# Kernel optimization log

Measured on AMD Instinct MI355X. Metric: run time of the kernel, lower is better.

The kernel has to match this reference:

```python
import jax, jax.numpy as jnp
import numpy as np

N_NODES = 50000


def gcn_conv(x, src, dst, W, b, n_nodes):
    """PyG GCNConv: linear -> sym-normalized aggregation with self-loops -> bias."""
    h = x @ W  # [N, out]
    # add self loops
    loop = jnp.arange(n_nodes, dtype=src.dtype)
    src_f = jnp.concatenate([src, loop])
    dst_f = jnp.concatenate([dst, loop])
    # degree at target nodes (edge weight = 1)
    deg = jax.ops.segment_sum(jnp.ones_like(dst_f, dtype=h.dtype), dst_f, num_segments=n_nodes)
    dinv = jnp.where(deg > 0, jax.lax.rsqrt(deg), 0.0)
    norm = dinv[src_f] * dinv[dst_f]  # [E+N]
    msg = h[src_f] * norm[:, None]    # gather + scale
    out = jax.ops.segment_sum(msg, dst_f, num_segments=n_nodes)
    return out + b


def setup_inputs() -> dict:
    key = jax.random.key(0)
    k1, k2, k3, k4 = jax.random.split(key, 4)
    N, F, H, C, E = N_NODES, 512, 256, 16, 800000
    x = jax.random.normal(k1, (N, F), dtype=jnp.float32)
    edge_index = jax.random.randint(k2, (2, E), 0, N, dtype=jnp.int64)
    W1 = jax.random.normal(k3, (F, H), dtype=jnp.float32) * (1.0 / np.sqrt(F))
    b1 = jnp.zeros((H,), dtype=jnp.float32)
    W2 = jax.random.normal(k4, (H, C), dtype=jnp.float32) * (1.0 / np.sqrt(H))
    b2 = jnp.zeros((C,), dtype=jnp.float32)
    return {"x": x, "edge_index": edge_index, "W1": W1, "b1": b1, "W2": W2, "b2": b2}


def reference(x, edge_index, W1, b1, W2, b2):
    src, dst = edge_index[0], edge_index[1]
    h = gcn_conv(x, src, dst, W1, b1, N_NODES)
    h = jax.nn.relu(h)
    # F.dropout with training=False (eval mode) is identity
    out = gcn_conv(h, src, dst, W2, b2, N_NODES)
    return out
```

## Files before the change

### kernel.cpp

```cpp
#include <hip/hip_runtime.h>
#include <stdint.h>

#define N_NODES 50000
#define N_PAD   50048
#define F_IN 512
#define H_DIM 256
#define C_DIM 16

typedef __attribute__((ext_vector_type(8))) short short8;
typedef __attribute__((ext_vector_type(4))) float f32x4;
typedef __attribute__((ext_vector_type(2))) float f32x2;
typedef __attribute__((ext_vector_type(4))) unsigned short us4;
typedef __attribute__((ext_vector_type(8))) unsigned short us8;

__device__ inline float bf2f(unsigned short u) {
    return __uint_as_float(((uint32_t)u) << 16);
}
__device__ inline unsigned short f2bf(float f) {
    uint32_t u = __float_as_uint(f);
    u += 0x7FFFu + ((u >> 16) & 1u);
    return (unsigned short)(u >> 16);
}
__device__ inline unsigned short hx(float f) {
    return (unsigned short)(__float_as_uint(f) >> 16);
}
__device__ inline int eidx(const void* p, long long i, int is64) {
    return is64 ? (int)((const long long*)p)[i] : ((const int*)p)[i];
}

#if __has_builtin(__builtin_amdgcn_cvt_pk_fp8_f32)
__device__ inline uint8_t f2fp8(float f) {
    int r = __builtin_amdgcn_cvt_pk_fp8_f32(f, f, 0, false);
    return (uint8_t)(r & 0xFF);
}
#else
__device__ inline uint8_t f2fp8(float f) {
    uint32_t u = __float_as_uint(f);
    uint32_t s = (u >> 24) & 0x80u;
    float a = fabsf(f);
    if (a >= 448.f) return (uint8_t)(s | 0x7E);
    if (a < 0.015625f) {
        int d = (int)rintf(a * 512.f);
        if (d < 8) return (uint8_t)(s | d);
        return (uint8_t)(s | 0x08);
    }
    uint32_t au = u & 0x7FFFFFFFu;
    uint32_t r = au + 0x7FFFFu + ((au >> 20) & 1u);
    uint32_t e = (r >> 23) - 120u;
    uint32_t m = (r >> 20) & 7u;
    if (e > 15u || (e == 15u && m == 7u)) return (uint8_t)(s | 0x7E);
    return (uint8_t)(s | (e << 3) | m);
}
#endif

#if __has_builtin(__builtin_amdgcn_cvt_pk_f32_fp8)
#define FP8CVT(w, hi) __builtin_amdgcn_cvt_pk_f32_fp8((w), (hi))
#else
__device__ inline float fp8b_to_f32(uint32_t v) {
    uint32_t e = (v >> 3) & 0xF, m = v & 7, s = (v >> 7) & 1;
    float r = e ? __uint_as_float(((e + 120u) << 23) | (m << 20))
                : (float)m * 0.001953125f;
    return s ? -r : r;
}
__device__ inline f32x2 FP8CVT(uint32_t w, bool hi) {
    uint32_t b = hi ? (w >> 16) : w;
    f32x2 r;
    r.x = fp8b_to_f32(b & 0xFF);
    r.y = fp8b_to_f32((b >> 8) & 0xFF);
    return r;
}
#endif

__device__ inline int row_beg(const int* ro, const int* bs, int n) {
    return ro[n] + bs[n >> 9];
}
__device__ inline int row_end(const int* ro, const int* bs, int n, int E) {
    return (n + 1 < N_NODES) ? ro[n + 1] + bs[(n + 1) >> 9] : E;
}

#define GLOAD16(gp, lp)                                                       \
    __builtin_amdgcn_global_load_lds(                                         \
        (const __attribute__((address_space(1))) void*)(gp),                  \
        (__attribute__((address_space(3))) void*)(lp), 16, 0, 0)


__global__ void prep_k(const void* ei, int* flag,
                       const float* w1, unsigned short* w1t,
                       const float* w2, unsigned short* w2t,
                       int* cnt, int* cur) {
    int i = blockIdx.x * 256 + threadIdx.x;
    if (i == 0) {
        const uint32_t* w = (const uint32_t*)ei;
        int is64 = 1;
        for (int j = 1; j < 128; j += 2)
            if (w[j] != 0u) { is64 = 0; break; }
        *flag = is64;
    }
    if (i < N_NODES) { cnt[i] = 0; cur[i] = 0; }
    if (i < F_IN * H_DIM) {
        int k = i / H_DIM, n = i % H_DIM;
        w1t[n * F_IN + k] = f2bf(w1[i]);
    }
    if (i < H_DIM * C_DIM) {
        int k = i / C_DIM, n = i % C_DIM;
        w2t[n * H_DIM + k] = f2bf(w2[i]);
    }
}


__global__ void hist_k(const void* ei, const int* flag, int* cnt, long long E) {
    long long e = (long long)blockIdx.x * 256 + threadIdx.x;
    if (e >= E) return;
    int d = eidx(ei, E + e, *flag);
    atomicAdd(&cnt[d], 1);
}

__global__ __launch_bounds__(512) void scan1_k(const int* cnt, int* rowoff, int* bsum,
                                               float* dinv, int n) {
    __shared__ int s[512];
    int t = threadIdx.x;
    int i = blockIdx.x * 512 + t;
    int v = (i < n) ? cnt[i] : 0;
    s[t] = v;
    __syncthreads();
    for (int off = 1; off < 512; off <<= 1) {
        int add = (t >= off) ? s[t - off] : 0;
        __syncthreads();
        s[t] += add;
        __syncthreads();
    }
    if (i < n) {
        rowoff[i] = s[t] - v;
        dinv[i] = rsqrtf((float)(v + 1));
    }
    if (t == 511) bsum[blockIdx.x] = s[511];
}

__global__ void scan2_k(int* bsum, int nb) {
    __shared__ int s[128];
    int t = threadIdx.x;
    int v = (t < nb) ? bsum[t] : 0;
    s[t] = v;
    __syncthreads();
    for (int off = 1; off < 128; off <<= 1) {
        int add = (t >= off) ? s[t - off] : 0;
        __syncthreads();
        s[t] += add;
        __syncthreads();
    }
    if (t < nb) bsum[t] = s[t] - v;
}

__global__ void scatter_k(const void* ei, const int* flag, const float* dinv,
                          const int* rowoff, const int* bsum, int* cur,
                          long long E, int2* colnorm) {
    long long e = (long long)blockIdx.x * 256 + threadIdx.x;
    if (e >= E) return;
    int is64 = *flag;
    int s = eidx(ei, e, is64);
    int d = eidx(ei, E + e, is64);
    int pos = row_beg(rowoff, bsum, d) + atomicAdd(&cur[d], 1);
    float nrm = dinv[s] * dinv[d];
    int2 cn;
    cn.x = s;
    cn.y = __float_as_int(nrm);
    colnorm[pos] = cn;
}


__global__ __launch_bounds__(512, 4) void gemm1_k(const float* __restrict__ x,
                                                  const unsigned short* __restrict__ w1t,
                                                  uint8_t* __restrict__ h1) {
    __shared__ __align__(16) float          Asf[2][128 * 32];
    __shared__ __align__(16) unsigned short Bs[2][256 * 32];

    const int t = threadIdx.x;
    const int wv = t >> 6, lane = t & 63;
    const int lg = lane >> 4, lr = lane & 15;
    const int wm = wv >> 2, wn = wv & 3;

    const int arow0 = t >> 3;
    const int achk = (t & 7) ^ (arow0 & 7);
    size_t g0 = (size_t)blockIdx.x * 128 + arow0;
    size_t g1 = g0 + 64;
    if (g0 > N_NODES - 1) g0 = N_NODES - 1;
    if (g1 > N_NODES - 1) g1 = N_NODES - 1;
    const float* asrc0 = x + g0 * F_IN + achk * 4;
    const float* asrc1 = x + g1 * F_IN + achk * 4;
    const unsigned short* bsrc0 = w1t + (size_t)(t >> 2) * F_IN + (t & 3) * 8;
    const unsigned short* bsrc1 = bsrc0 + 128 * F_IN;

#define STAGE(bf, ks)                                                         \
    do { const int _o = (ks) * 32;                                            \
        GLOAD16(asrc0 + _o, &Asf[bf][t * 4]);                                 \
        GLOAD16(asrc1 + _o, &Asf[bf][t * 4 + 2048]);                          \
        GLOAD16(bsrc0 + _o, &Bs[bf][t * 8]);                                  \
        GLOAD16(bsrc1 + _o, &Bs[bf][(t + 512) * 8]);                          \
    } while (0)

    f32x4 acc[4][4] = {};

    STAGE(0, 0);

    for (int ks = 0; ks < 16; ++ks) {
        const int bf = ks & 1;
        if (ks < 15) {
            STAGE(bf ^ 1, ks + 1);
            asm volatile("s_waitcnt vmcnt(4)" ::: "memory");
        } else {
            asm volatile("s_waitcnt vmcnt(0)" ::: "memory");
        }
        __builtin_amdgcn_sched_barrier(0);
        __builtin_amdgcn_s_barrier();

        short8 afr[4], bfr[4];
#pragma unroll
        for (int mi = 0; mi < 4; ++mi) {
            const int r = wm * 64 + mi * 16 + lr;
            const int s = r & 7;
            const float* base = &Asf[bf][r * 32];
            f32x4 lo = *(const f32x4*)(base + (((lg * 2) ^ s) * 4));
            f32x4 hi = *(const f32x4*)(base + (((lg * 2 + 1) ^ s) * 4));
            short8 a;
            a[0] = (short)hx(lo[0]); a[1] = (short)hx(lo[1]);
            a[2] = (short)hx(lo[2]); a[3] = (short)hx(lo[3]);
            a[4] = (short)hx(hi[0]); a[5] = (short)hx(hi[1]);
            a[6] = (short)hx(hi[2]); a[7] = (short)hx(hi[3]);
            afr[mi] = a;
        }
#pragma unroll
        for (int ni = 0; ni < 4; ++ni)
            bfr[ni] = *(const short8*)&Bs[bf][(wn * 64 + ni * 16 + lr) * 32 + lg * 8];
#pragma unroll
        for (int mi = 0; mi < 4; ++mi)
#pragma unroll
            for (int ni = 0; ni < 4; ++ni)
                acc[mi][ni] = __builtin_amdgcn_mfma_f32_16x16x32_bf16(
                    afr[mi], bfr[ni], acc[mi][ni], 0, 0, 0);

        asm volatile("s_waitcnt lgkmcnt(0)" ::: "memory");
        __builtin_amdgcn_sched_barrier(0);
        __builtin_amdgcn_s_barrier();
    }
#undef STAGE

    const size_t rbase = (size_t)blockIdx.x * 128 + wm * 64 + lg * 4;
#pragma unroll
    for (int mi = 0; mi < 4; ++mi)
#pragma unroll
        for (int ni = 0; ni < 4; ++ni) {
            const int col = wn * 64 + ni * 16 + lr;
#pragma unroll
            for (int j = 0; j < 4; ++j)
                h1[(rbase + mi * 16 + j) * H_DIM + col] = f2fp8(acc[mi][ni][j]);
        }
}


__global__ __launch_bounds__(256) void agg1_k(const uint8_t* __restrict__ h1,
                                              const int* __restrict__ rowoff,
                                              const int* __restrict__ bsum,
                                              const int2* __restrict__ colnorm,
                                              const float* __restrict__ dinv,
                                              const float* __restrict__ b1,
                                              unsigned short* __restrict__ h1a,
                                              int E) {
    int wv = threadIdx.x >> 6, lane = threadIdx.x & 63;
    int node = blockIdx.x * 4 + wv;
    if (node >= N_NODES) return;
    int half = lane >> 5;
    int fl = (lane & 31) * 8;
    int beg = row_beg(rowoff, bsum, node);
    int end = row_end(rowoff, bsum, node, E);
    float a[8] = {0.f, 0.f, 0.f, 0.f, 0.f, 0.f, 0.f, 0.f};
    const uint8_t* base = h1 + fl;

#define ACCUM(vv, nn)                                                         \
    do { f32x2 p0 = FP8CVT((vv).x, false), p1 = FP8CVT((vv).x, true);         \
         f32x2 p2 = FP8CVT((vv).y, false), p3 = FP8CVT((vv).y, true);         \
         a[0] += (nn) * p0.x; a[1] += (nn) * p0.y;                            \
         a[2] += (nn) * p1.x; a[3] += (nn) * p1.y;                            \
         a[4] += (nn) * p2.x; a[5] += (nn) * p2.y;                            \
         a[6] += (nn) * p3.x; a[7] += (nn) * p3.y; } while (0)

    int e = beg + half;
    while (e + 6 < end) {
        int2 c[4];
        uint2 v[4];
#pragma unroll
        for (int q = 0; q < 4; ++q) c[q] = colnorm[e + q * 2];
#pragma unroll
        for (int q = 0; q < 4; ++q)
            v[q] = *(const uint2*)(base + (size_t)c[q].x * H_DIM);
#pragma unroll
        for (int q = 0; q < 4; ++q) {
            float n = __int_as_float(c[q].y);
            ACCUM(v[q], n);
        }
        e += 8;
    }
    while (e < end) {
        int2 c0 = colnorm[e];
        uint2 v0 = *(const uint2*)(base + (size_t)c0.x * H_DIM);
        float n0 = __int_as_float(c0.y);
        ACCUM(v0, n0);
        e += 2;
    }
#undef ACCUM
#pragma unroll
    for (int j = 0; j < 8; ++j)
        a[j] += __shfl_xor(a[j], 32);

    if (half == 0) {
        float dn = dinv[node];
        float sn = dn * dn;
        uint2 vsv = *(const uint2*)(base + (size_t)node * H_DIM);
        f32x2 s0 = FP8CVT(vsv.x, false), s1 = FP8CVT(vsv.x, true);
        f32x2 s2 = FP8CVT(vsv.y, false), s3 = FP8CVT(vsv.y, true);
        float sv[8] = {s0.x, s0.y, s1.x, s1.y, s2.x, s2.y, s3.x, s3.y};
        float4 b0 = *(const float4*)(b1 + fl);
        float4 b4 = *(const float4*)(b1 + fl + 4);
        float bb[8] = {b0.x, b0.y, b0.z, b0.w, b4.x, b4.y, b4.z, b4.w};
        us8 o;
#pragma unroll
        for (int j = 0; j < 8; ++j) {
            float r = fmaxf(a[j] + sn * sv[j] + bb[j], 0.f);
            o[j] = f2bf(r);
        }
        *(us8*)(h1a + (long long)node * H_DIM + fl) = o;
    }
}


__global__ __launch_bounds__(256) void gemm2_k(const unsigned short* __restrict__ h1a,
                                               const unsigned short* __restrict__ w2t,
                                               float* __restrict__ h2) {
    int t = threadIdx.x;
    int wv = t >> 6, lane = t & 63, lg = lane >> 4, lr = lane & 15;
    int rbase = blockIdx.x * 64 + wv * 16;
    int rr = rbase + lr;
    int rc = rr < N_NODES ? rr : N_NODES - 1;
    f32x4 acc = {0.f, 0.f, 0.f, 0.f};
#pragma unroll
    for (int ks = 0; ks < 8; ++ks) {
        short8 a = *(const short8*)(h1a + (long long)rc * H_DIM + ks * 32 + lg * 8);
        short8 b = *(const short8*)(w2t + lr * H_DIM + ks * 32 + lg * 8);
        acc = __builtin_amdgcn_mfma_f32_16x16x32_bf16(a, b, acc, 0, 0, 0);
    }
#pragma unroll
    for (int j = 0; j < 4; ++j) {
        int row = rbase + lg * 4 + j;
        if (row < N_NODES) h2[(long long)row * C_DIM + lr] = acc[j];
    }
}


__global__ __launch_bounds__(256) void agg2_k(const float* __restrict__ h2,
                                              const int* __restrict__ rowoff,
                                              const int* __restrict__ bsum,
                                              const int2* __restrict__ colnorm,
                                              const float* __restrict__ dinv,
                                              const float* __restrict__ b2,
                                              float* __restrict__ out, int E) {
    int g = threadIdx.x >> 4, c = threadIdx.x & 15;
    int node = blockIdx.x * 16 + g;
    if (node >= N_NODES) return;
    int beg = row_beg(rowoff, bsum, node);
    int end = row_end(rowoff, bsum, node, E);
    float acc = 0.f;
    int e = beg;
    for (; e + 3 < end; e += 4) {
        int2 cn0 = colnorm[e];
        int2 cn1 = colnorm[e + 1];
        int2 cn2 = colnorm[e + 2];
        int2 cn3 = colnorm[e + 3];
        float v0 = h2[(long long)cn0.x * C_DIM + c];
        float v1 = h2[(long long)cn1.x * C_DIM + c];
        float v2 = h2[(long long)cn2.x * C_DIM + c];
        float v3 = h2[(long long)cn3.x * C_DIM + c];
        acc += __int_as_float(cn0.y) * v0 + __int_as_float(cn1.y) * v1
             + __int_as_float(cn2.y) * v2 + __int_as_float(cn3.y) * v3;
    }
    for (; e < end; ++e) {
        int2 cn = colnorm[e];
        acc += __int_as_float(cn.y) * h2[(long long)cn.x * C_DIM + c];
    }
    float dn = dinv[node];
    acc += dn * dn * h2[(long long)node * C_DIM + c];
    out[(long long)node * C_DIM + c] = acc + b2[c];
}


extern "C" void kernel_launch(void* const* d_in, const int* in_sizes, int n_in,
                              void* d_out, int out_size, void* d_ws, size_t ws_size,
                              hipStream_t stream) {
    const float* x  = (const float*)d_in[0];
    const void*  ei = d_in[1];
    const float* W1 = (const float*)d_in[2];
    const float* b1 = (const float*)d_in[3];
    const float* W2 = (const float*)d_in[4];
    const float* b2 = (const float*)d_in[5];
    float* out = (float*)d_out;
    long long E = (long long)in_sizes[1] / 2;

    char* w = (char*)d_ws;
    auto alloc = [&](size_t bytes) -> char* {
        char* p = w;
        w += (bytes + 255) & ~(size_t)255;
        return p;
    };
    int*   flag    = (int*)   alloc(4);
    int*   cnt     = (int*)   alloc((size_t)N_NODES * 4);
    int*   cur     = (int*)   alloc((size_t)N_NODES * 4);
    float* dinv    = (float*) alloc((size_t)N_NODES * 4);
    int*   rowoff  = (int*)   alloc((size_t)N_NODES * 4);
    int*   bsum    = (int*)   alloc(512 * 4);
    int2*  colnorm = (int2*)  alloc((size_t)E * 8);
    unsigned short* w1t = (unsigned short*)alloc((size_t)H_DIM * F_IN * 2);
    unsigned short* w2t = (unsigned short*)alloc((size_t)C_DIM * H_DIM * 2);
    uint8_t* h1 = (uint8_t*)alloc((size_t)N_PAD * H_DIM);
    unsigned short* h1a = (unsigned short*)alloc((size_t)N_NODES * H_DIM * 2);
    float* h2 = (float*)alloc((size_t)N_NODES * C_DIM * 4);

    prep_k<<<(F_IN * H_DIM + 255) / 256, 256, 0, stream>>>(ei, flag, W1, w1t, W2, w2t,
                                                           cnt, cur);

    int egrid = (int)((E + 255) / 256);
    hist_k<<<egrid, 256, 0, stream>>>(ei, flag, cnt, E);
    int sgrid = (N_NODES + 511) / 512;
    scan1_k<<<sgrid, 512, 0, stream>>>(cnt, rowoff, bsum, dinv, N_NODES);
    scan2_k<<<1, 128, 0, stream>>>(bsum, sgrid);
    scatter_k<<<egrid, 256, 0, stream>>>(ei, flag, dinv, rowoff, bsum, cur, E, colnorm);

    gemm1_k<<<N_PAD / 128, 512, 0, stream>>>(x, w1t, h1);
    agg1_k<<<(N_NODES + 3) / 4, 256, 0, stream>>>(h1, rowoff, bsum, colnorm, dinv,
                                                  b1, h1a, (int)E);
    gemm2_k<<<(N_NODES + 63) / 64, 256, 0, stream>>>(h1a, w2t, h2);
    agg2_k<<<(N_NODES + 15) / 16, 256, 0, stream>>>(h2, rowoff, bsum, colnorm, dinv,
                                                    b2, out, (int)E);
}
```

Before: 181.4 us.

## Fold block-sum scan into scatter, process two edges per thread, widen agg2 per node

Removes the separate single-block scan2 launch by having every scatter block redo the small 98-entry block-sum scan in shared memory, with block 0 writing the exclusive result to a new bscan buffer that the aggregation kernels read. The hist and scatter kernels now handle two edges per thread, halving their grids. agg2 moves from 16 lanes per node to a full wavefront per node, splitting edges across four lane groups and combining them with shuffles. This trades redundant per-block scan work and lower node-per-block density in agg2 for one fewer launch and more memory-level parallelism on high-degree rows.

```diff
diff --git a/kernel.cpp b/kernel.cpp
--- a/kernel.cpp
+++ b/kernel.cpp
@@ -6,6 +6,7 @@
 #define F_IN 512
 #define H_DIM 256
 #define C_DIM 16
+#define NCHUNK ((N_NODES + 511) / 512)
 
 typedef __attribute__((ext_vector_type(8))) short short8;
 typedef __attribute__((ext_vector_type(4))) float f32x4;
@@ -109,10 +110,12 @@
 
 
 __global__ void hist_k(const void* ei, const int* flag, int* cnt, long long E) {
-    long long e = (long long)blockIdx.x * 256 + threadIdx.x;
+    long long e = ((long long)blockIdx.x * 256 + threadIdx.x) * 2;
     if (e >= E) return;
-    int d = eidx(ei, E + e, *flag);
-    atomicAdd(&cnt[d], 1);
+    int is64 = *flag;
+    atomicAdd(&cnt[eidx(ei, E + e, is64)], 1);
+    if (e + 1 < E)
+        atomicAdd(&cnt[eidx(ei, E + e + 1, is64)], 1);
 }
 
 __global__ __launch_bounds__(512) void scan1_k(const int* cnt, int* rowoff, int* bsum,
@@ -136,35 +139,44 @@
     if (t == 511) bsum[blockIdx.x] = s[511];
 }
 
-__global__ void scan2_k(int* bsum, int nb) {
-    __shared__ int s[128];
-    int t = threadIdx.x;
-    int v = (t < nb) ? bsum[t] : 0;
-    s[t] = v;
+
+__global__ __launch_bounds__(256) void scatter_k(const void* ei, const int* flag,
+                                                 const float* dinv,
+                                                 const int* rowoff, const int* bsum,
+                                                 int* bscan, int* cur,
+                                                 long long E, int2* colnorm) {
+    __shared__ int sb[128];
+    const int t = threadIdx.x;
+    if (t < 128) sb[t] = (t < NCHUNK) ? bsum[t] : 0;
     __syncthreads();
+#pragma unroll
     for (int off = 1; off < 128; off <<= 1) {
-        int add = (t >= off) ? s[t - off] : 0;
+        int add = (t < 128 && t >= off) ? sb[t - off] : 0;
         __syncthreads();
-        s[t] += add;
+        if (t < 128) sb[t] += add;
         __syncthreads();
     }
-    if (t < nb) bsum[t] = s[t] - v;
-}
-
-__global__ void scatter_k(const void* ei, const int* flag, const float* dinv,
-                          const int* rowoff, const int* bsum, int* cur,
-                          long long E, int2* colnorm) {
-    long long e = (long long)blockIdx.x * 256 + threadIdx.x;
-    if (e >= E) return;
-    int is64 = *flag;
-    int s = eidx(ei, e, is64);
-    int d = eidx(ei, E + e, is64);
-    int pos = row_beg(rowoff, bsum, d) + atomicAdd(&cur[d], 1);
-    float nrm = dinv[s] * dinv[d];
-    int2 cn;
-    cn.x = s;
-    cn.y = __float_as_int(nrm);
-    colnorm[pos] = cn;
+    int ex = 0;
+    if (t < 128) ex = (t == 0) ? 0 : sb[t - 1];
+    __syncthreads();
+    if (t < 128) sb[t] = ex;
+    __syncthreads();
+    if (blockIdx.x == 0 && t < NCHUNK) bscan[t] = sb[t];
+
+    const int is64 = *flag;
+    long long e = ((long long)blockIdx.x * 256 + t) * 2;
+#pragma unroll
+    for (int q = 0; q < 2; ++q, ++e) {
+        if (e >= E) break;
+        int s = eidx(ei, e, is64);
+        int d = eidx(ei, E + e, is64);
+        int pos = rowoff[d] + sb[d >> 9] + atomicAdd(&cur[d], 1);
+        float nrm = dinv[s] * dinv[d];
+        int2 cn;
+        cn.x = s;
+        cn.y = __float_as_int(nrm);
+        colnorm[pos] = cn;
+    }
 }
 
 
@@ -259,7 +271,7 @@
 
 __global__ __launch_bounds__(256) void agg1_k(const uint8_t* __restrict__ h1,
                                               const int* __restrict__ rowoff,
-                                              const int* __restrict__ bsum,
+                                              const int* __restrict__ bscan,
                                               const int2* __restrict__ colnorm,
                                               const float* __restrict__ dinv,
                                               const float* __restrict__ b1,
@@ -270,8 +282,8 @@
     if (node >= N_NODES) return;
     int half = lane >> 5;
     int fl = (lane & 31) * 8;
-    int beg = row_beg(rowoff, bsum, node);
-    int end = row_end(rowoff, bsum, node, E);
+    int beg = row_beg(rowoff, bscan, node);
+    int end = row_end(rowoff, bscan, node, E);
     float a[8] = {0.f, 0.f, 0.f, 0.f, 0.f, 0.f, 0.f, 0.f};
     const uint8_t* base = h1 + fl;
 
@@ -357,37 +369,39 @@
 
 __global__ __launch_bounds__(256) void agg2_k(const float* __restrict__ h2,
                                               const int* __restrict__ rowoff,
-                                              const int* __restrict__ bsum,
+                                              const int* __restrict__ bscan,
                                               const int2* __restrict__ colnorm,
                                               const float* __restrict__ dinv,
                                               const float* __restrict__ b2,
                                               float* __restrict__ out, int E) {
-    int g = threadIdx.x >> 4, c = threadIdx.x & 15;
-    int node = blockIdx.x * 16 + g;
+    int wv = threadIdx.x >> 6, lane = threadIdx.x & 63;
+    int node = blockIdx.x * 4 + wv;
     if (node >= N_NODES) return;
-    int beg = row_beg(rowoff, bsum, node);
-    int end = row_end(rowoff, bsum, node, E);
+    int eg = lane >> 4, c = lane & 15;
+    int beg = row_beg(rowoff, bscan, node);
+    int end = row_end(rowoff, bscan, node, E);
     float acc = 0.f;
-    int e = beg;
-    for (; e + 3 < end; e += 4) {
-        int2 cn0 = colnorm[e];
-        int2 cn1 = colnorm[e + 1];
-        int2 cn2 = colnorm[e + 2];
-        int2 cn3 = colnorm[e + 3];
-        float v0 = h2[(long long)cn0.x * C_DIM + c];
-        float v1 = h2[(long long)cn1.x * C_DIM + c];
-        float v2 = h2[(long long)cn2.x * C_DIM + c];
-        float v3 = h2[(long long)cn3.x * C_DIM + c];
-        acc += __int_as_float(cn0.y) * v0 + __int_as_float(cn1.y) * v1
-             + __int_as_float(cn2.y) * v2 + __int_as_float(cn3.y) * v3;
-    }
-    for (; e < end; ++e) {
-        int2 cn = colnorm[e];
-        acc += __int_as_float(cn.y) * h2[(long long)cn.x * C_DIM + c];
-    }
-    float dn = dinv[node];
-    acc += dn * dn * h2[(long long)node * C_DIM + c];
-    out[(long long)node * C_DIM + c] = acc + b2[c];
+    int e = beg + eg;
+    while (e + 4 < end) {
+        int2 c0 = colnorm[e];
+        int2 c1 = colnorm[e + 4];
+        float v0 = h2[(size_t)c0.x * C_DIM + c];
+        float v1 = h2[(size_t)c1.x * C_DIM + c];
+        acc += __int_as_float(c0.y) * v0 + __int_as_float(c1.y) * v1;
+        e += 8;
+    }
+    while (e < end) {
+        int2 c0 = colnorm[e];
+        acc += __int_as_float(c0.y) * h2[(size_t)c0.x * C_DIM + c];
+        e += 4;
+    }
+    acc += __shfl_xor(acc, 16);
+    acc += __shfl_xor(acc, 32);
+    if (eg == 0) {
+        float dn = dinv[node];
+        acc += dn * dn * h2[(size_t)node * C_DIM + c] + b2[c];
+        out[(size_t)node * C_DIM + c] = acc;
+    }
 }
 
 
@@ -415,6 +429,7 @@
     float* dinv    = (float*) alloc((size_t)N_NODES * 4);
     int*   rowoff  = (int*)   alloc((size_t)N_NODES * 4);
     int*   bsum    = (int*)   alloc(512 * 4);
+    int*   bscan   = (int*)   alloc(512 * 4);
     int2*  colnorm = (int2*)  alloc((size_t)E * 8);
     unsigned short* w1t = (unsigned short*)alloc((size_t)H_DIM * F_IN * 2);
     unsigned short* w2t = (unsigned short*)alloc((size_t)C_DIM * H_DIM * 2);
@@ -425,17 +440,16 @@
     prep_k<<<(F_IN * H_DIM + 255) / 256, 256, 0, stream>>>(ei, flag, W1, w1t, W2, w2t,
                                                            cnt, cur);
 
-    int egrid = (int)((E + 255) / 256);
-    hist_k<<<egrid, 256, 0, stream>>>(ei, flag, cnt, E);
-    int sgrid = (N_NODES + 511) / 512;
-    scan1_k<<<sgrid, 512, 0, stream>>>(cnt, rowoff, bsum, dinv, N_NODES);
-    scan2_k<<<1, 128, 0, stream>>>(bsum, sgrid);
-    scatter_k<<<egrid, 256, 0, stream>>>(ei, flag, dinv, rowoff, bsum, cur, E, colnorm);
+    int e2grid = (int)((E / 2 + 255) / 256);
+    hist_k<<<e2grid, 256, 0, stream>>>(ei, flag, cnt, E);
+    scan1_k<<<NCHUNK, 512, 0, stream>>>(cnt, rowoff, bsum, dinv, N_NODES);
+    scatter_k<<<e2grid, 256, 0, stream>>>(ei, flag, dinv, rowoff, bsum, bscan, cur,
+                                          E, colnorm);
 
     gemm1_k<<<N_PAD / 128, 512, 0, stream>>>(x, w1t, h1);
-    agg1_k<<<(N_NODES + 3) / 4, 256, 0, stream>>>(h1, rowoff, bsum, colnorm, dinv,
+    agg1_k<<<(N_NODES + 3) / 4, 256, 0, stream>>>(h1, rowoff, bscan, colnorm, dinv,
                                                   b1, h1a, (int)E);
     gemm2_k<<<(N_NODES + 63) / 64, 256, 0, stream>>>(h1a, w2t, h2);
-    agg2_k<<<(N_NODES + 15) / 16, 256, 0, stream>>>(h2, rowoff, bsum, colnorm, dinv,
-                                                    b2, out, (int)E);
-}
+    agg2_k<<<(N_NODES + 3) / 4, 256, 0, stream>>>(h2, rowoff, bscan, colnorm, dinv,
+                                                  b2, out, (int)E);
+}
```

Result: slower. 188.8 us (+4.1%).
